# Performance work log

Hardware: AMD Instinct MI355X
Metric: run time of the kernel (lower is better)

Reference implementation:

```python
import jax, jax.numpy as jnp
import numpy as np

N, E, W, H, NXF, NDF = 131072, 8, 128, 64, 10, 4
DX = 3 + 3 * 2 * NXF  # 63
DV = 3 + 3 * 2 * NDF  # 27
TEMP = 0.166667


def pe(x, degree):
    # positional encoding: [x, sin(2^i x), cos(2^i x)]
    y = jnp.concatenate([(2.0 ** i) * x for i in range(degree)], -1)
    return jnp.concatenate([x, jnp.sin(y), jnp.cos(y)], -1)


def setup_inputs() -> dict:
    key = jax.random.key(0)
    ks = jax.random.split(key, 8)
    s = 0.05
    return {
        'x': jax.random.normal(ks[0], (N, 6), jnp.float32),
        'W_enc': jax.random.normal(ks[1], (DX, W), jnp.float32) * s,
        'b_enc': jnp.zeros((W,), jnp.float32),
        'W_sh': jax.random.normal(ks[2], (E, W, W), jnp.float32) * s,
        'b_sh': jnp.zeros((E, W), jnp.float32),
        'w_sig': jax.random.normal(ks[3], (W,), jnp.float32) * s,
        'b_sig': jnp.zeros((1,), jnp.float32),
        'W_r1': jax.random.normal(ks[4], (E, W + DV, H), jnp.float32) * s,
        'b_r1': jnp.zeros((E, H), jnp.float32),
        'W_r2': jax.random.normal(ks[5], (E, H, 3), jnp.float32) * s,
        'b_r2': jnp.zeros((E, 3), jnp.float32),
    }


def reference(x, W_enc, b_enc, W_sh, b_sh, w_sig, b_sig, W_r1, b_r1, W_r2, b_r2):
    xyz = pe(x[:, :3], NXF)          # [N, 63]
    vd = pe(x[:, 3:6], NDF)          # [N, 27]
    y = jax.nn.relu(xyz @ W_enc + b_enc)  # encoding_xyz -> [N, W]
    # all shape experts at once: [N, E, W]
    shape_out = jax.nn.relu(jnp.einsum('nd,edh->neh', y, W_sh) + b_sh)
    # shared sigma head, softplus keeps sigma > 0: [N, E]
    sigmas = jax.nn.softplus(jnp.einsum('neh,h->ne', shape_out, w_sig) + b_sig)
    log_logits = jax.nn.log_softmax(jnp.log(sigmas + 1e-10) / TEMP, axis=-1)
    # gumbel-softmax (tau=1, torch default) with fixed noise key
    u = jax.random.uniform(jax.random.key(42), sigmas.shape, jnp.float32)
    g = -jnp.log(-jnp.log(u + 1e-20) + 1e-20)
    gates_soft = jax.nn.softmax(log_logits + g, axis=-1)
    index = jnp.argmax(gates_soft, axis=-1)  # [N]
    hard = jax.nn.one_hot(index, E, dtype=sigmas.dtype)
    # straight-through hard gates
    gates_hard = hard - jax.lax.stop_gradient(gates_soft) + gates_soft
    sigmas_pooled = jnp.take_along_axis(sigmas, index[:, None], axis=-1)  # [N, 1]
    # rgb experts: concat(shape_out_i, viewdir) -> MLP -> sigmoid rgb, gated sum
    vdb = jnp.broadcast_to(vd[:, None, :], (vd.shape[0], E, DV))
    inp = jnp.concatenate([shape_out, vdb], axis=-1)  # [N, E, W+27]
    h = jax.nn.relu(jnp.einsum('nec,ech->neh', inp, W_r1) + b_r1)
    rgb = jax.nn.sigmoid(jnp.einsum('neh,eho->neo', h, W_r2) + b_r2)  # [N, E, 3]
    rgbs = jnp.sum(rgb * gates_hard[:, :, None], axis=1)  # [N, 3]
    return jnp.concatenate([rgbs, sigmas_pooled], axis=-1)  # [N, 4]
```

## Files before the change

### kernel.cpp

```cpp
#include <hip/hip_runtime.h>
#include <hip/hip_bf16.h>


#define NPTS 131072
#define PT 64
#define NTH 256
#define NBLK (NPTS / PT)
#define INV2048 (1.0f / 2048.0f)

#define WS_ENC_H 0
#define WS_ENC_L 8192
#define WS_SH_H  16384
#define WS_SH_L  147456
#define WS_R1_H  278528

#define OFF_YH   0
#define OFF_B    17408
#define OFF_GUM  35840
#define OFF_RED  38912
#define OFF_LIST (OFF_RED + 0)
#define OFF_CNT  (OFF_RED + 256)
#define OFF_OFFS (OFF_RED + 288)
#define OFF_BID  (OFF_RED + 320)
#define SMEM_SZ  47104

typedef __attribute__((ext_vector_type(8))) _Float16 f16x8;
typedef __attribute__((ext_vector_type(4))) _Float16 f16x4;
typedef __attribute__((ext_vector_type(4))) float f32x4;

#define MFMA(a, b, c) __builtin_amdgcn_mfma_f32_16x16x32_f16((a), (b), (c), 0, 0, 0)

__device__ __forceinline__ unsigned rotl32(unsigned x, int d) {
  return (x << d) | (x >> (32 - d));
}

__device__ __forceinline__ float gumbel_for(unsigned flat) {
  const unsigned k0 = 0u, k1 = 42u;
  const unsigned ks2 = k0 ^ k1 ^ 0x1BD11BDAu;
  unsigned x0 = 0u + k0;
  unsigned x1 = flat + k1;
#define TF_RND(r) { x0 += x1; x1 = rotl32(x1, r); x1 ^= x0; }
  TF_RND(13) TF_RND(15) TF_RND(26) TF_RND(6)
  x0 += k1;  x1 += ks2 + 1u;
  TF_RND(17) TF_RND(29) TF_RND(16) TF_RND(24)
  x0 += ks2; x1 += k0 + 2u;
  TF_RND(13) TF_RND(15) TF_RND(26) TF_RND(6)
  x0 += k0;  x1 += k1 + 3u;
  TF_RND(17) TF_RND(29) TF_RND(16) TF_RND(24)
  x0 += k1;  x1 += ks2 + 4u;
  TF_RND(13) TF_RND(15) TF_RND(26) TF_RND(6)
  x0 += ks2; x1 += k0 + 5u;
#undef TF_RND
  unsigned bits = x0 ^ x1;
  float u = __uint_as_float((bits >> 9) | 0x3f800000u) - 1.0f;
  return -logf(-logf(u + 1e-20f) + 1e-20f);
}

__global__ void prep_kernel(const float* __restrict__ W_enc,
                            const float* __restrict__ W_sh,
                            const float* __restrict__ W_r1,
                            _Float16* __restrict__ ws) {
  int idx = blockIdx.x * 256 + threadIdx.x;
  if (idx < 8192) {
    int tile = idx >> 9, r = idx & 511;
    int L = r >> 3, j = r & 7;
    int nt = tile >> 1, kt = tile & 1;
    int k = kt * 32 + (L >> 4) * 8 + j;
    int n = nt * 16 + (L & 15);
    float v = (k < 63) ? W_enc[k * 128 + n] : 0.0f;
    _Float16 h = (_Float16)v;
    ws[WS_ENC_H + idx] = h;
    ws[WS_ENC_L + idx] = (_Float16)((v - (float)h) * 2048.0f);
  } else if (idx < 8192 + 131072) {
    int s = idx - 8192;
    int tile = s >> 9, r = s & 511;
    int L = r >> 3, j = r & 7;
    int e = tile >> 5, nt = (tile >> 2) & 7, kt = tile & 3;
    int k = kt * 32 + (L >> 4) * 8 + j;
    int n = nt * 16 + (L & 15);
    float v = W_sh[e * 16384 + k * 128 + n];
    _Float16 h = (_Float16)v;
    ws[WS_SH_H + s] = h;
    ws[WS_SH_L + s] = (_Float16)((v - (float)h) * 2048.0f);
  } else if (idx < 8192 + 131072 + 81920) {
    int s = idx - (8192 + 131072);
    int tile = s >> 9, r = s & 511;
    int L = r >> 3, j = r & 7;
    int e = tile / 20, rr = tile % 20;
    int nt = rr / 5, kt = rr % 5;
    int k = kt * 32 + (L >> 4) * 8 + j;
    int n = nt * 16 + (L & 15);
    float v = (k < 155) ? W_r1[e * 9920 + k * 64 + n] : 0.0f;
    ws[WS_R1_H + s] = (_Float16)v;
  }
}

__global__ __launch_bounds__(NTH, 2)
void nerf_moe_kernel(const float* __restrict__ x,
                     const float* __restrict__ b_enc,
                     const float* __restrict__ b_sh,
                     const float* __restrict__ w_sig, const float* __restrict__ b_sig,
                     const float* __restrict__ b_r1,
                     const float* __restrict__ W_r2,  const float* __restrict__ b_r2,
                     const _Float16* __restrict__ wsw,
                     float* __restrict__ out) {
  __shared__ __align__(16) unsigned char smem[SMEM_SZ];
  _Float16* sYh  = (_Float16*)(smem + OFF_YH);
  float*    sH   = (float*)(smem + OFF_YH);
  _Float16* sYl  = (_Float16*)(smem + OFF_B);
  _Float16* sPEh = (_Float16*)(smem + OFF_B);
  _Float16* sPEl = (_Float16*)(smem + OFF_B + 9216);
  _Float16* sSB  = (_Float16*)(smem + OFF_B);
  float*    sRedE = (float*)(smem + OFF_RED);
  float*    sGum = (float*)(smem + OFF_GUM);
  int*      sBid = (int*)(smem + OFF_BID);
  int*      sList = (int*)(smem + OFF_LIST);
  int*      sCnt = (int*)(smem + OFF_CNT);
  int*      sOff = (int*)(smem + OFF_OFFS);

  const int t  = threadIdx.x;
  const int w  = t >> 6;
  const int L  = t & 63;
  const int q  = L >> 4;
  const int c  = L & 15;
  const int n0 = blockIdx.x * PT;

  for (int idx = t; idx < PT * 64; idx += NTH) {
    int p = idx >> 6, f = idx & 63;
    const float* xr = x + (size_t)(n0 + p) * 6;
    float v;
    if (f < 3)       v = xr[f];
    else if (f < 33) { int g = f - 3;  v = sinf(xr[g % 3] * (float)(1 << (g / 3))); }
    else if (f < 63) { int g = f - 33; v = cosf(xr[g % 3] * (float)(1 << (g / 3))); }
    else             v = 0.0f;
    _Float16 h = (_Float16)v;
    sPEh[p * 72 + f] = h;
    sPEl[p * 72 + f] = (_Float16)((v - (float)h) * 2048.0f);
  }
  sGum[t]       = gumbel_for((unsigned)(n0 * 8 + t));
  sGum[t + 256] = gumbel_for((unsigned)(n0 * 8 + t + 256));
  __syncthreads();

  {
    f16x8 beh[2][2], bel[2][2];
    #pragma unroll
    for (int ntL = 0; ntL < 2; ++ntL)
      #pragma unroll
      for (int kt = 0; kt < 2; ++kt) {
        int tile = (2 * w + ntL) * 2 + kt;
        beh[ntL][kt] = *(const f16x8*)(wsw + WS_ENC_H + tile * 512 + L * 8);
        bel[ntL][kt] = *(const f16x8*)(wsw + WS_ENC_L + tile * 512 + L * 8);
      }
    f16x8 pah[4][2], pal[4][2];
    #pragma unroll
    for (int mt = 0; mt < 4; ++mt)
      #pragma unroll
      for (int kt = 0; kt < 2; ++kt) {
        int off = (mt * 16 + c) * 72 + kt * 32 + q * 8;
        pah[mt][kt] = *(const f16x8*)(sPEh + off);
        pal[mt][kt] = *(const f16x8*)(sPEl + off);
      }
    f32x4 a1[4][2], a2[4][2];
    #pragma unroll
    for (int mt = 0; mt < 4; ++mt)
      #pragma unroll
      for (int ntL = 0; ntL < 2; ++ntL) { a1[mt][ntL] = (f32x4)0.0f; a2[mt][ntL] = (f32x4)0.0f; }
    #pragma unroll
    for (int kt = 0; kt < 2; ++kt)
      #pragma unroll
      for (int mt = 0; mt < 4; ++mt)
        #pragma unroll
        for (int ntL = 0; ntL < 2; ++ntL) {
          a1[mt][ntL] = MFMA(pah[mt][kt], beh[ntL][kt], a1[mt][ntL]);
          a2[mt][ntL] = MFMA(pah[mt][kt], bel[ntL][kt], a2[mt][ntL]);
          a2[mt][ntL] = MFMA(pal[mt][kt], beh[ntL][kt], a2[mt][ntL]);
        }
    __syncthreads();
    float bb0 = b_enc[(2 * w) * 16 + c];
    float bb1 = b_enc[(2 * w + 1) * 16 + c];
    #pragma unroll
    for (int mt = 0; mt < 4; ++mt)
      #pragma unroll
      for (int ntL = 0; ntL < 2; ++ntL) {
        float bb = ntL ? bb1 : bb0;
        int col = (2 * w + ntL) * 16 + c;
        #pragma unroll
        for (int r = 0; r < 4; ++r) {
          float v = fmaxf(a1[mt][ntL][r] + a2[mt][ntL][r] * INV2048 + bb, 0.0f);
          int row = mt * 16 + q * 4 + r;
          _Float16 h = (_Float16)v;
          sYh[row * 136 + col] = h;
          sYl[row * 136 + col] = (_Float16)((v - (float)h) * 2048.0f);
        }
      }
  }
  __syncthreads();

  f16x8 Ah[4][4];
  #pragma unroll
  for (int nt = 0; nt < 4; ++nt)
    #pragma unroll
    for (int kt = 0; kt < 4; ++kt)
      Ah[nt][kt] = *(const f16x8*)(sYh + (nt * 16 + c) * 136 + kt * 32 + q * 8);
  const f32x4 wsv0 = *(const f32x4*)(w_sig + (2 * w) * 16 + q * 4);
  const f32x4 wsv1 = *(const f32x4*)(w_sig + (2 * w + 1) * 16 + q * 4);

  #pragma unroll 1
  for (int e = 0; e < 8; ++e) {
    float psum[4] = {0.f, 0.f, 0.f, 0.f};
    #pragma unroll
    for (int i = 0; i < 2; ++i) {
      f32x4 a1[4], a2[4];
      #pragma unroll
      for (int nt = 0; nt < 4; ++nt) { a1[nt] = (f32x4)0.0f; a2[nt] = (f32x4)0.0f; }
      #pragma unroll
      for (int kt = 0; kt < 4; ++kt) {
        int tile = (e * 8 + 2 * w + i) * 4 + kt;
        f16x8 bh = *(const f16x8*)(wsw + WS_SH_H + tile * 512 + L * 8);
        f16x8 bl = *(const f16x8*)(wsw + WS_SH_L + tile * 512 + L * 8);
        #pragma unroll
        for (int nt = 0; nt < 4; ++nt) {
          f16x8 al = *(const f16x8*)(sYl + (nt * 16 + c) * 136 + kt * 32 + q * 8);
          a1[nt] = MFMA(bh, Ah[nt][kt], a1[nt]);
          a2[nt] = MFMA(bl, Ah[nt][kt], a2[nt]);
          a2[nt] = MFMA(bh, al, a2[nt]);
        }
      }
      f32x4 bb = *(const f32x4*)(b_sh + e * 128 + (2 * w + i) * 16 + q * 4);
      f32x4 wv = i ? wsv1 : wsv0;
      #pragma unroll
      for (int nt = 0; nt < 4; ++nt)
        #pragma unroll
        for (int r = 0; r < 4; ++r) {
          float s = fmaxf(fmaf(a2[nt][r], INV2048, a1[nt][r]) + bb[r], 0.0f);
          psum[nt] = fmaf(s, wv[r], psum[nt]);
        }
    }
    #pragma unroll
    for (int nt = 0; nt < 4; ++nt) {
      float v = psum[nt];
      v += __shfl_xor(v, 16);
      v += __shfl_xor(v, 32);
      psum[nt] = v;
    }
    if (q == 0) {
      #pragma unroll
      for (int nt = 0; nt < 4; ++nt)
        sRedE[e * 256 + w * 64 + nt * 16 + c] = psum[nt];
    }
  }
  __syncthreads();

  if (t < PT) {
    float best = 0.0f, bsig = 0.0f;
    int bide = 0;
    const float bs = b_sig[0];
    #pragma unroll
    for (int e = 0; e < 8; ++e) {
      const float* rp = sRedE + e * 256 + t;
      float s = (rp[0] + rp[64]) + (rp[128] + rp[192]);
      float dotv = s + bs;
      float sig = fmaxf(dotv, 0.0f) + log1pf(expf(-fabsf(dotv)));
      float z = logf(sig + 1e-10f) / 0.166667f;
      float score = z + sGum[t * 8 + e];
      if (e == 0 || score > best) { best = score; bsig = sig; bide = e; }
    }
    sBid[t] = bide;
    out[(size_t)(n0 + t) * 4 + 3] = bsig;
  }
  __syncthreads();

  if (t < 8) {
    int cnt = 0;
    for (int p = 0; p < PT; ++p) cnt += (sBid[p] == t);
    sCnt[t] = cnt;
  }
  __syncthreads();
  if (t < 8) {
    int off = 0;
    for (int i = 0; i < t; ++i) off += sCnt[i];
    sOff[t] = off;
    int k = off;
    for (int p = 0; p < PT; ++p) if (sBid[p] == t) sList[k++] = p;
  }
  __syncthreads();

  for (int idx = t; idx < PT * 32; idx += NTH) {
    int s = idx >> 5, cc = idx & 31;
    int pt = sList[s];
    const float* xr = x + (size_t)(n0 + pt) * 6 + 3;
    float v;
    if (cc < 3)       v = xr[cc];
    else if (cc < 15) { int g = cc - 3;  v = sinf(xr[g % 3] * (float)(1 << (g / 3))); }
    else if (cc < 27) { int g = cc - 15; v = cosf(xr[g % 3] * (float)(1 << (g / 3))); }
    else              v = 0.0f;
    sSB[s * 168 + 128 + cc] = (_Float16)v;
  }
  #pragma unroll 1
  for (int ei = 0; ei < 2; ++ei) {
    int e = 2 * w + ei;
    int cnt = sCnt[e], off = sOff[e];
    for (int base = 0; base < cnt; base += 16) {
      int sidx = base + c; if (sidx >= cnt) sidx = cnt - 1;
      int pt = sList[off + sidx];
      f16x8 yb[4];
      #pragma unroll
      for (int kt = 0; kt < 4; ++kt)
        yb[kt] = *(const f16x8*)(sYh + pt * 136 + kt * 32 + q * 8);
      f32x4 acc[8];
      #pragma unroll
      for (int jt = 0; jt < 8; ++jt) acc[jt] = (f32x4)0.0f;
      #pragma unroll
      for (int jt = 0; jt < 8; ++jt)
        #pragma unroll
        for (int kt = 0; kt < 4; ++kt) {
          f16x8 a = *(const f16x8*)(wsw + WS_SH_H + ((e * 8 + jt) * 4 + kt) * 512 + L * 8);
          acc[jt] = MFMA(a, yb[kt], acc[jt]);
        }
      bool wr = (base + c) < cnt;
      int slot = off + base + c;
      #pragma unroll
      for (int jt = 0; jt < 8; ++jt) {
        f32x4 bb = *(const f32x4*)(b_sh + e * 128 + jt * 16 + q * 4);
        f16x4 v;
        #pragma unroll
        for (int r = 0; r < 4; ++r)
          v[r] = (_Float16)fmaxf(acc[jt][r] + bb[r], 0.0f);
        if (wr) *(f16x4*)(sSB + slot * 168 + jt * 16 + q * 4) = v;
      }
    }
  }
  __syncthreads();

  #pragma unroll 1
  for (int ei = 0; ei < 2; ++ei) {
    int e = 2 * w + ei;
    int cnt = sCnt[e], off = sOff[e];
    for (int base = 0; base < cnt; base += 16) {
      int sidx = base + c; if (sidx >= cnt) sidx = cnt - 1;
      int slot = off + sidx;
      f16x8 ag[5];
      #pragma unroll
      for (int kt = 0; kt < 5; ++kt)
        ag[kt] = *(const f16x8*)(sSB + slot * 168 + kt * 32 + q * 8);
      f32x4 hacc[4];
      #pragma unroll
      for (int nt = 0; nt < 4; ++nt) hacc[nt] = (f32x4)0.0f;
      #pragma unroll
      for (int nt = 0; nt < 4; ++nt)
        #pragma unroll
        for (int kt = 0; kt < 5; ++kt) {
          f16x8 bf = *(const f16x8*)(wsw + WS_R1_H + ((e * 4 + nt) * 5 + kt) * 512 + L * 8);
          hacc[nt] = MFMA(ag[kt], bf, hacc[nt]);
        }
      #pragma unroll
      for (int nt = 0; nt < 4; ++nt) {
        float bb = b_r1[e * 64 + nt * 16 + c];
        #pragma unroll
        for (int r = 0; r < 4; ++r) {
          int m = q * 4 + r;
          if (base + m < cnt)
            sH[(off + base + m) * 68 + nt * 16 + c] = fmaxf(hacc[nt][r] + bb, 0.0f);
        }
      }
    }
  }
  __syncthreads();

  if (t < 192) {
    int s = t / 3, o = t - s * 3;
    int pt = sList[s];
    int e = sBid[pt];
    float a = b_r2[e * 3 + o];
    const float* w2 = W_r2 + e * 192 + o;
    #pragma unroll
    for (int jj = 0; jj < 64; jj += 4) {
      f32x4 h4 = *(const f32x4*)(sH + s * 68 + jj);
      a = fmaf(h4.x, w2[jj * 3], a);
      a = fmaf(h4.y, w2[jj * 3 + 3], a);
      a = fmaf(h4.z, w2[jj * 3 + 6], a);
      a = fmaf(h4.w, w2[jj * 3 + 9], a);
    }
    out[(size_t)(n0 + pt) * 4 + o] = 1.0f / (1.0f + expf(-a));
  }
}

extern "C" void kernel_launch(void* const* d_in, const int* in_sizes, int n_in,
                              void* d_out, int out_size, void* d_ws, size_t ws_size,
                              hipStream_t stream) {
  (void)in_sizes; (void)n_in; (void)ws_size; (void)out_size;
  const float* x     = (const float*)d_in[0];
  const float* W_enc = (const float*)d_in[1];
  const float* b_enc = (const float*)d_in[2];
  const float* W_sh  = (const float*)d_in[3];
  const float* b_sh  = (const float*)d_in[4];
  const float* w_sig = (const float*)d_in[5];
  const float* b_sig = (const float*)d_in[6];
  const float* W_r1  = (const float*)d_in[7];
  const float* b_r1  = (const float*)d_in[8];
  const float* W_r2  = (const float*)d_in[9];
  const float* b_r2  = (const float*)d_in[10];
  _Float16* ws = (_Float16*)d_ws;
  float* outp = (float*)d_out;
  prep_kernel<<<864, 256, 0, stream>>>(W_enc, W_sh, W_r1, ws);
  nerf_moe_kernel<<<NBLK, NTH, 0, stream>>>(x, b_enc, b_sh, w_sig, b_sig,
                                            b_r1, W_r2, b_r2, ws, outp);
}
```

Baseline: 278.5 us.

## Software-pipeline shape-expert weight loads and parallelize gating across all threads

The per-expert shape loop is fully unrolled into 16 steps, with the next step's hi/lo weight tiles and bias loaded into double-buffered registers while the current step's MFMAs run. This is meant to hide global/L2 load latency behind compute. Gating now uses all 256 threads (4 per point, 2 experts each, combined with shuffles), and the Gumbel noise is computed inline instead of precomputed into shared memory. The small index arrays are moved into padding slots of the shared buffer. The cost is higher register pressure from the full unroll and double buffers, which could hurt occupancy at 2 blocks per CU.

Measured after the change: 278.3 us. No clear change (-0.1%).

```diff
diff --git a/kernel.cpp b/kernel.cpp
--- a/kernel.cpp
+++ b/kernel.cpp
@@ -16,13 +16,13 @@
 
 #define OFF_YH   0
 #define OFF_B    17408
-#define OFF_GUM  35840
 #define OFF_RED  38912
-#define OFF_LIST (OFF_RED + 0)
-#define OFF_CNT  (OFF_RED + 256)
-#define OFF_OFFS (OFF_RED + 288)
-#define OFF_BID  (OFF_RED + 320)
 #define SMEM_SZ  47104
+
+#define S_LIST(s) (*(int*)(smem + OFF_B + (s) * 336 + 320))
+#define S_BID(p)  (*(int*)(smem + OFF_B + (p) * 336 + 324))
+#define S_CNT(e)  (*(int*)(smem + OFF_B + (e) * 336 + 328))
+#define S_OFF(e)  (*(int*)(smem + OFF_B + (e) * 336 + 332))
 
 typedef __attribute__((ext_vector_type(8))) _Float16 f16x8;
 typedef __attribute__((ext_vector_type(4))) _Float16 f16x4;
@@ -112,11 +112,6 @@
   _Float16* sPEl = (_Float16*)(smem + OFF_B + 9216);
   _Float16* sSB  = (_Float16*)(smem + OFF_B);
   float*    sRedE = (float*)(smem + OFF_RED);
-  float*    sGum = (float*)(smem + OFF_GUM);
-  int*      sBid = (int*)(smem + OFF_BID);
-  int*      sList = (int*)(smem + OFF_LIST);
-  int*      sCnt = (int*)(smem + OFF_CNT);
-  int*      sOff = (int*)(smem + OFF_OFFS);
 
   const int t  = threadIdx.x;
   const int w  = t >> 6;
@@ -137,8 +132,6 @@
     sPEh[p * 72 + f] = h;
     sPEl[p * 72 + f] = (_Float16)((v - (float)h) * 2048.0f);
   }
-  sGum[t]       = gumbel_for((unsigned)(n0 * 8 + t));
-  sGum[t + 256] = gumbel_for((unsigned)(n0 * 8 + t + 256));
   __syncthreads();
 
   {
@@ -205,89 +198,119 @@
   const f32x4 wsv0 = *(const f32x4*)(w_sig + (2 * w) * 16 + q * 4);
   const f32x4 wsv1 = *(const f32x4*)(w_sig + (2 * w + 1) * 16 + q * 4);
 
-  #pragma unroll 1
-  for (int e = 0; e < 8; ++e) {
-    float psum[4] = {0.f, 0.f, 0.f, 0.f};
-    #pragma unroll
-    for (int i = 0; i < 2; ++i) {
-      f32x4 a1[4], a2[4];
-      #pragma unroll
-      for (int nt = 0; nt < 4; ++nt) { a1[nt] = (f32x4)0.0f; a2[nt] = (f32x4)0.0f; }
-      #pragma unroll
-      for (int kt = 0; kt < 4; ++kt) {
-        int tile = (e * 8 + 2 * w + i) * 4 + kt;
-        f16x8 bh = *(const f16x8*)(wsw + WS_SH_H + tile * 512 + L * 8);
-        f16x8 bl = *(const f16x8*)(wsw + WS_SH_L + tile * 512 + L * 8);
-        #pragma unroll
-        for (int nt = 0; nt < 4; ++nt) {
-          f16x8 al = *(const f16x8*)(sYl + (nt * 16 + c) * 136 + kt * 32 + q * 8);
-          a1[nt] = MFMA(bh, Ah[nt][kt], a1[nt]);
-          a2[nt] = MFMA(bl, Ah[nt][kt], a2[nt]);
-          a2[nt] = MFMA(bh, al, a2[nt]);
-        }
-      }
-      f32x4 bb = *(const f32x4*)(b_sh + e * 128 + (2 * w + i) * 16 + q * 4);
-      f32x4 wv = i ? wsv1 : wsv0;
-      #pragma unroll
-      for (int nt = 0; nt < 4; ++nt)
-        #pragma unroll
-        for (int r = 0; r < 4; ++r) {
-          float s = fmaxf(fmaf(a2[nt][r], INV2048, a1[nt][r]) + bb[r], 0.0f);
-          psum[nt] = fmaf(s, wv[r], psum[nt]);
-        }
-    }
-    #pragma unroll
-    for (int nt = 0; nt < 4; ++nt) {
-      float v = psum[nt];
-      v += __shfl_xor(v, 16);
-      v += __shfl_xor(v, 32);
-      psum[nt] = v;
-    }
-    if (q == 0) {
-      #pragma unroll
-      for (int nt = 0; nt < 4; ++nt)
-        sRedE[e * 256 + w * 64 + nt * 16 + c] = psum[nt];
-    }
-  }
-  __syncthreads();
-
-  if (t < PT) {
-    float best = 0.0f, bsig = 0.0f;
+  float psum[4] = {0.f, 0.f, 0.f, 0.f};
+
+  auto LOADW = [&](int s, f16x8 bh[4], f16x8 bl[4], f32x4& bb) {
+    int e = s >> 1, i = s & 1;
+    int tbase = (e * 8 + 2 * w + i) * 4;
+    #pragma unroll
+    for (int kt = 0; kt < 4; ++kt) {
+      bh[kt] = *(const f16x8*)(wsw + WS_SH_H + (tbase + kt) * 512 + L * 8);
+      bl[kt] = *(const f16x8*)(wsw + WS_SH_L + (tbase + kt) * 512 + L * 8);
+    }
+    bb = *(const f32x4*)(b_sh + e * 128 + (2 * w + i) * 16 + q * 4);
+  };
+
+  auto STEP = [&](int s, const f16x8 bh[4], const f16x8 bl[4], const f32x4& bb) {
+    f32x4 a1[4], a2[4];
+    #pragma unroll
+    for (int nt = 0; nt < 4; ++nt) { a1[nt] = (f32x4)0.0f; a2[nt] = (f32x4)0.0f; }
+    #pragma unroll
+    for (int kt = 0; kt < 4; ++kt)
+      #pragma unroll
+      for (int nt = 0; nt < 4; ++nt) {
+        f16x8 al = *(const f16x8*)(sYl + (nt * 16 + c) * 136 + kt * 32 + q * 8);
+        a1[nt] = MFMA(bh[kt], Ah[nt][kt], a1[nt]);
+        a2[nt] = MFMA(bl[kt], Ah[nt][kt], a2[nt]);
+        a2[nt] = MFMA(bh[kt], al, a2[nt]);
+      }
+    f32x4 wv = (s & 1) ? wsv1 : wsv0;
+    #pragma unroll
+    for (int nt = 0; nt < 4; ++nt)
+      #pragma unroll
+      for (int r = 0; r < 4; ++r) {
+        float sv = fmaxf(fmaf(a2[nt][r], INV2048, a1[nt][r]) + bb[r], 0.0f);
+        psum[nt] = fmaf(sv, wv[r], psum[nt]);
+      }
+    if (s & 1) {
+      int e = s >> 1;
+      #pragma unroll
+      for (int nt = 0; nt < 4; ++nt) {
+        float v = psum[nt];
+        v += __shfl_xor(v, 16);
+        v += __shfl_xor(v, 32);
+        if (q == 0) sRedE[e * 256 + w * 64 + nt * 16 + c] = v;
+        psum[nt] = 0.f;
+      }
+    }
+  };
+
+  {
+    f16x8 bh0[4], bl0[4], bh1[4], bl1[4];
+    f32x4 bb0, bb1;
+    LOADW(0, bh0, bl0, bb0);
+    #pragma unroll
+    for (int s = 0; s < 16; ++s) {
+      if ((s & 1) == 0) {
+        if (s + 1 < 16) LOADW(s + 1, bh1, bl1, bb1);
+        STEP(s, bh0, bl0, bb0);
+      } else {
+        if (s + 1 < 16) LOADW(s + 1, bh0, bl0, bb0);
+        STEP(s, bh1, bl1, bb1);
+      }
+    }
+  }
+  __syncthreads();
+
+  {
+    int pt = t >> 2;
+    int eb = (t & 3) * 2;
+    float best = -1e30f, bsig = 0.0f;
     int bide = 0;
     const float bs = b_sig[0];
     #pragma unroll
-    for (int e = 0; e < 8; ++e) {
-      const float* rp = sRedE + e * 256 + t;
+    for (int j = 0; j < 2; ++j) {
+      int e = eb + j;
+      const float* rp = sRedE + e * 256 + pt;
       float s = (rp[0] + rp[64]) + (rp[128] + rp[192]);
       float dotv = s + bs;
       float sig = fmaxf(dotv, 0.0f) + log1pf(expf(-fabsf(dotv)));
       float z = logf(sig + 1e-10f) / 0.166667f;
-      float score = z + sGum[t * 8 + e];
-      if (e == 0 || score > best) { best = score; bsig = sig; bide = e; }
-    }
-    sBid[t] = bide;
-    out[(size_t)(n0 + t) * 4 + 3] = bsig;
+      float score = z + gumbel_for((unsigned)((n0 + pt) * 8 + e));
+      if (score > best) { best = score; bsig = sig; bide = e; }
+    }
+    #pragma unroll
+    for (int m = 1; m <= 2; m <<= 1) {
+      float oS  = __shfl_xor(best, m);
+      float oSg = __shfl_xor(bsig, m);
+      int   oI  = __shfl_xor(bide, m);
+      if (oS > best || (oS == best && oI < bide)) { best = oS; bsig = oSg; bide = oI; }
+    }
+    if ((t & 3) == 0) {
+      S_BID(pt) = bide;
+      out[(size_t)(n0 + pt) * 4 + 3] = bsig;
+    }
   }
   __syncthreads();
 
   if (t < 8) {
     int cnt = 0;
-    for (int p = 0; p < PT; ++p) cnt += (sBid[p] == t);
-    sCnt[t] = cnt;
+    for (int p = 0; p < PT; ++p) cnt += (S_BID(p) == t);
+    S_CNT(t) = cnt;
   }
   __syncthreads();
   if (t < 8) {
     int off = 0;
-    for (int i = 0; i < t; ++i) off += sCnt[i];
-    sOff[t] = off;
+    for (int i = 0; i < t; ++i) off += S_CNT(i);
+    S_OFF(t) = off;
     int k = off;
-    for (int p = 0; p < PT; ++p) if (sBid[p] == t) sList[k++] = p;
+    for (int p = 0; p < PT; ++p) if (S_BID(p) == t) { S_LIST(k) = p; k++; }
   }
   __syncthreads();
 
   for (int idx = t; idx < PT * 32; idx += NTH) {
     int s = idx >> 5, cc = idx & 31;
-    int pt = sList[s];
+    int pt = S_LIST(s);
     const float* xr = x + (size_t)(n0 + pt) * 6 + 3;
     float v;
     if (cc < 3)       v = xr[cc];
@@ -299,10 +322,10 @@
   #pragma unroll 1
   for (int ei = 0; ei < 2; ++ei) {
     int e = 2 * w + ei;
-    int cnt = sCnt[e], off = sOff[e];
+    int cnt = S_CNT(e), off = S_OFF(e);
     for (int base = 0; base < cnt; base += 16) {
       int sidx = base + c; if (sidx >= cnt) sidx = cnt - 1;
-      int pt = sList[off + sidx];
+      int pt = S_LIST(off + sidx);
       f16x8 yb[4];
       #pragma unroll
       for (int kt = 0; kt < 4; ++kt)
@@ -335,7 +358,7 @@
   #pragma unroll 1
   for (int ei = 0; ei < 2; ++ei) {
     int e = 2 * w + ei;
-    int cnt = sCnt[e], off = sOff[e];
+    int cnt = S_CNT(e), off = S_OFF(e);
     for (int base = 0; base < cnt; base += 16) {
       int sidx = base + c; if (sidx >= cnt) sidx = cnt - 1;
       int slot = off + sidx;
@@ -369,8 +392,8 @@
 
   if (t < 192) {
     int s = t / 3, o = t - s * 3;
-    int pt = sList[s];
-    int e = sBid[pt];
+    int pt = S_LIST(s);
+    int e = S_BID(pt);
     float a = b_r2[e * 3 + o];
     const float* w2 = W_r2 + e * 192 + o;
     #pragma unroll
```
